# Optimization experiments

Hardware: AMD Instinct MI355X
Metric: run time of the kernel (lower is better)

Reference implementation:

```python
import jax, jax.numpy as jnp
import numpy as np

DIM = 1024
NUM_HEADS = 16
HEAD_DIM = DIM // NUM_HEADS
SCALE = HEAD_DIM ** -0.5


def setup_inputs() -> dict:
    key = jax.random.key(0)
    ks = jax.random.split(key, 6)
    B, N = 2, 2048
    s = DIM ** -0.5
    return {
        "x": jax.random.normal(ks[0], (B, N, DIM), dtype=jnp.float32),
        "Wq": jax.random.normal(ks[1], (DIM, DIM), dtype=jnp.float32) * s,
        "Wk": jax.random.normal(ks[2], (DIM, DIM), dtype=jnp.float32) * s,
        "Wv": jax.random.normal(ks[3], (DIM, DIM), dtype=jnp.float32) * s,
        "Wp": jax.random.normal(ks[4], (DIM, DIM), dtype=jnp.float32) * s,
        "bp": jax.random.normal(ks[5], (DIM,), dtype=jnp.float32) * 0.01,
    }


def reference(x, Wq, Wk, Wv, Wp, bp):
    B, N, C = x.shape
    H, D = NUM_HEADS, HEAD_DIM
    # projections (torch Linear: x @ W.T); reshape to (B, H, N, D)
    q = (x @ Wq.T).reshape(B, N, H, D).transpose(0, 2, 1, 3)
    k = (x @ Wk.T).reshape(B, N, H, D).transpose(0, 2, 1, 3)
    v = (x @ Wv.T).reshape(B, N, H, D).transpose(0, 2, 1, 3)
    attn = jnp.einsum("bhnd,bhmd->bhnm", q, k) * SCALE
    attn = jax.nn.softmax(attn, axis=-1)  # dropout p=0 -> identity
    out = jnp.einsum("bhnm,bhmd->bhnd", attn, v)
    out = out.transpose(0, 2, 1, 3).reshape(B, N, C)
    return out @ Wp.T + bp
```

## Files before the change

kernel.cpp:

```cpp
#include <hip/hip_runtime.h>
#include <cstdint>

#define DIMC   1024
#define NHEADS 16
#define HD     64
#define BATCH  2
#define SEQ    2048
#define MROWS  (BATCH*SEQ)
#define QSCALE2 0.18033688f

typedef __bf16 bf16x8 __attribute__((ext_vector_type(8)));
typedef float  f32x4  __attribute__((ext_vector_type(4)));

#define AST 88
#define TST 136

__device__ __forceinline__ unsigned short f2bf(float f) {
    union { float f; unsigned int u; } v; v.f = f;
    unsigned int u = v.u;
    u += 0x7fffu + ((u >> 16) & 1u);
    return (unsigned short)(u >> 16);
}

__device__ __forceinline__ unsigned int pk2bf(float a, float b) {
    union { float f; unsigned int u; } ua, ub;
    ua.f = a; ub.f = b;
    return __builtin_amdgcn_perm(ub.u + 0x8000u, ua.u + 0x8000u, 0x07060302u);
}

__device__ __forceinline__ void gload_lds16(const void* g, void* l) {
    __builtin_amdgcn_global_load_lds(
        (const __attribute__((address_space(1))) unsigned int*)g,
        (__attribute__((address_space(3))) unsigned int*)l, 16, 0, 0);
}

__global__ __launch_bounds__(256) void cast_all(
    const float* __restrict__ x,
    const float* __restrict__ Wq, const float* __restrict__ Wk,
    const float* __restrict__ Wv, const float* __restrict__ Wp,
    unsigned short* __restrict__ xb, unsigned short* __restrict__ Wb)
{
    const size_t M1 = (size_t)DIMC * DIMC;
    int y = blockIdx.y;
    const float* src;
    unsigned short* dst;
    if (y < 4)      { src = x  + (size_t)y * M1; dst = xb + (size_t)y * M1; }
    else if (y == 4){ src = Wq; dst = Wb; }
    else if (y == 5){ src = Wk; dst = Wb + M1; }
    else if (y == 6){ src = Wv; dst = Wb + 2 * M1; }
    else            { src = Wp; dst = Wb + 3 * M1; }
    size_t idx = ((size_t)blockIdx.x * 256 + threadIdx.x) * 4;
    float4 v = *(const float4*)(src + idx);
    ushort4 p; p.x = f2bf(v.x); p.y = f2bf(v.y); p.z = f2bf(v.z); p.w = f2bf(v.w);
    *(ushort4*)(dst + idx) = p;
}

__device__ __forceinline__ void gemm_issue(
    const unsigned short* __restrict__ A, const unsigned short* __restrict__ B,
    unsigned short* As, unsigned short* Bs, int m0, int n0, int kt)
{
    const int t = threadIdx.x;
    const int w = t >> 6, lane = t & 63;
    const int srow = lane >> 3, scol = lane & 7;
#pragma unroll
    for (int i = 0; i < 4; ++i) {
        int r  = i * 32 + w * 8 + srow;
        int cg = scol ^ (r & 7);
        gload_lds16(A + (size_t)(m0 + r) * DIMC + kt + cg * 8, As + r * 64 + scol * 8);
        gload_lds16(B + (size_t)(n0 + r) * DIMC + kt + cg * 8, Bs + r * 64 + scol * 8);
    }
}

__device__ __forceinline__ void gemm_compute(
    const unsigned short* As, const unsigned short* Bs, f32x4 acc[4][4])
{
    const int t = threadIdx.x;
    const int w = t >> 6, lane = t & 63, quad = lane >> 4, lr = lane & 15;
    const int wr = w >> 1, wc = w & 1;
#pragma unroll
    for (int kk = 0; kk < 2; ++kk) {
        bf16x8 af[4], bfr[4];
#pragma unroll
        for (int mt = 0; mt < 4; ++mt) {
            int row = wr * 64 + mt * 16 + lr;
            int cb  = kk * 4 + quad;
            af[mt] = *(const bf16x8*)&As[row * 64 + (cb ^ (row & 7)) * 8];
        }
#pragma unroll
        for (int nt = 0; nt < 4; ++nt) {
            int row = wc * 64 + nt * 16 + lr;
            int cb  = kk * 4 + quad;
            bfr[nt] = *(const bf16x8*)&Bs[row * 64 + (cb ^ (row & 7)) * 8];
        }
#pragma unroll
        for (int mt = 0; mt < 4; ++mt)
#pragma unroll
            for (int nt = 0; nt < 4; ++nt)
                acc[mt][nt] = __builtin_amdgcn_mfma_f32_16x16x32_bf16(af[mt], bfr[nt], acc[mt][nt], 0, 0, 0);
    }
}

__device__ __forceinline__ void gemm_k_loop_db(
    const unsigned short* __restrict__ A, const unsigned short* __restrict__ B,
    unsigned short* smem, int m0, int n0, f32x4 acc[4][4])
{
    unsigned short* As0 = smem;
    unsigned short* Bs0 = smem + 8192;
    unsigned short* As1 = smem + 16384;
    unsigned short* Bs1 = smem + 24576;

    gemm_issue(A, B, As0, Bs0, m0, n0, 0);
    for (int kt = 0; kt < DIMC; kt += 128) {
        __syncthreads();
        gemm_issue(A, B, As1, Bs1, m0, n0, kt + 64);
        gemm_compute(As0, Bs0, acc);
        __syncthreads();
        if (kt + 128 < DIMC) gemm_issue(A, B, As0, Bs0, m0, n0, kt + 128);
        gemm_compute(As1, Bs1, acc);
    }
}

__device__ __forceinline__ void vt_epilogue(
    unsigned short* Ts, f32x4 acc[4][4], int m0, int n0,
    unsigned short* __restrict__ vT)
{
    const int t = threadIdx.x;
    const int w = t >> 6, lane = t & 63, quad = lane >> 4, lr = lane & 15;
    const int wr = w >> 1, wc = w & 1;

    __syncthreads();
#pragma unroll
    for (int mt = 0; mt < 4; ++mt)
#pragma unroll
        for (int nt = 0; nt < 4; ++nt) {
            int lcol  = wc * 64 + nt * 16 + lr;
            int lrow0 = wr * 64 + mt * 16 + quad * 4;
            ushort4 p;
            p.x = f2bf(acc[mt][nt][0]); p.y = f2bf(acc[mt][nt][1]);
            p.z = f2bf(acc[mt][nt][2]); p.w = f2bf(acc[mt][nt][3]);
            *(ushort4*)&Ts[lcol * TST + lrow0] = p;
        }
    __syncthreads();

    int lc = t >> 1, half = t & 1;
    int cg = n0 + lc, hh = cg >> 6, dd = cg & 63;
    int bb = m0 >> 11, nn0 = m0 & (SEQ - 1);
    size_t dst = ((size_t)((bb * NHEADS + hh) * HD + dd)) * SEQ + nn0 + half * 64;
    const unsigned short* srcp = &Ts[lc * TST + half * 64];
#pragma unroll
    for (int i = 0; i < 8; ++i)
        *(uint4*)&vT[dst + i * 8] = *(const uint4*)&srcp[i * 8];
}

__global__ __launch_bounds__(256) void gemm_qkv_fast(
    const unsigned short* __restrict__ xb, const unsigned short* __restrict__ Wb,
    unsigned short* __restrict__ qo, unsigned short* __restrict__ ko,
    unsigned short* __restrict__ vT)
{
    __shared__ unsigned short smem[32768];

    const int t  = threadIdx.x;
    const int n0 = blockIdx.x * 128, m0 = blockIdx.y * 128, z = blockIdx.z;
    const unsigned short* B = Wb + (size_t)z * DIMC * DIMC;
    const int w = t >> 6, lane = t & 63, quad = lane >> 4, lr = lane & 15;
    const int wr = w >> 1, wc = w & 1;

    f32x4 acc[4][4];
#pragma unroll
    for (int mt = 0; mt < 4; ++mt)
#pragma unroll
        for (int nt = 0; nt < 4; ++nt)
#pragma unroll
            for (int r = 0; r < 4; ++r) acc[mt][nt][r] = 0.f;

    gemm_k_loop_db(xb, B, smem, m0, n0, acc);

    if (z == 2) {
        vt_epilogue(smem, acc, m0, n0, vT);
    } else {
        unsigned short* Out = (z == 0) ? qo : ko;
        const float sc = (z == 0) ? QSCALE2 : 1.0f;
#pragma unroll
        for (int mt = 0; mt < 4; ++mt)
#pragma unroll
            for (int nt = 0; nt < 4; ++nt)
#pragma unroll
                for (int r = 0; r < 4; ++r) {
                    int row = m0 + wr * 64 + mt * 16 + quad * 4 + r;
                    int col = n0 + wc * 64 + nt * 16 + lr;
                    Out[(size_t)row * DIMC + col] = f2bf(acc[mt][nt][r] * sc);
                }
    }
}

__global__ __launch_bounds__(256) void gemm_out_fast(
    const unsigned short* __restrict__ O, const unsigned short* __restrict__ Wpb,
    const float* __restrict__ bias, float* __restrict__ out)
{
    __shared__ unsigned short smem[32768];

    const int t  = threadIdx.x;
    const int n0 = blockIdx.x * 128, m0 = blockIdx.y * 128;
    const int w = t >> 6, lane = t & 63, quad = lane >> 4, lr = lane & 15;
    const int wr = w >> 1, wc = w & 1;

    f32x4 acc[4][4];
#pragma unroll
    for (int mt = 0; mt < 4; ++mt)
#pragma unroll
        for (int nt = 0; nt < 4; ++nt)
#pragma unroll
            for (int r = 0; r < 4; ++r) acc[mt][nt][r] = 0.f;

    gemm_k_loop_db(O, Wpb, smem, m0, n0, acc);

#pragma unroll
    for (int mt = 0; mt < 4; ++mt)
#pragma unroll
        for (int nt = 0; nt < 4; ++nt)
#pragma unroll
            for (int r = 0; r < 4; ++r) {
                int row = m0 + wr * 64 + mt * 16 + quad * 4 + r;
                int col = n0 + wc * 64 + nt * 16 + lr;
                out[(size_t)row * DIMC + col] = acc[mt][nt][r] + bias[col];
            }
}

__global__ __launch_bounds__(256, 4) void attn_kernel(
    const unsigned short* __restrict__ qg, const unsigned short* __restrict__ kg,
    const unsigned short* __restrict__ vT, unsigned short* __restrict__ og)
{
    __shared__ unsigned short Ka[64 * 64];
    __shared__ unsigned short Kb[64 * 64];
    __shared__ unsigned short Va[64 * 64];
    __shared__ unsigned short Vb[64 * 64];
    __shared__ unsigned short Ps[64 * 64];

    const int t  = threadIdx.x;
    const int w = t >> 6, l = t & 63, quad = l >> 4, lr = l & 15;
    const int srow = t >> 3, scol = t & 7;
    const int pkey = (lr & 7) << 1;

    const int bid  = blockIdx.x;
    const int slot = bid >> 3;
    const int bh   = (bid & 7) * 4 + (slot >> 5);
    const int qt   = slot & 31;
    const int b    = bh >> 4, h = bh & 15;

    const unsigned short* khead = kg + ((size_t)(b * SEQ)) * DIMC + h * HD;
    const unsigned short* vhead = vT + (size_t)((b * NHEADS + h) * HD) * SEQ;

    bf16x8 qf[2];
    {
        const size_t qoff = ((size_t)(b * SEQ + qt * 64 + w * 16 + lr)) * DIMC + h * HD;
        qf[0] = *(const bf16x8*)(qg + qoff + 0  + quad * 8);
        qf[1] = *(const bf16x8*)(qg + qoff + 32 + quad * 8);
    }

    bf16x8 ones;
#pragma unroll
    for (int j = 0; j < 8; ++j) ones[j] = (__bf16)1.0f;
    const f32x4 fzero = { 0.f, 0.f, 0.f, 0.f };

    f32x4 o_acc[4], lacc;
    lacc = fzero;
#pragma unroll
    for (int ct = 0; ct < 4; ++ct) o_acc[ct] = fzero;

    auto issue = [&](int kt, unsigned short* Kd, unsigned short* Vd) {
#pragma unroll
        for (int i = 0; i < 2; ++i) {
            int r  = i * 32 + srow;
            int cg = scol ^ (r & 7);
            gload_lds16(khead + (size_t)(kt * 64 + r) * DIMC + cg * 8, Kd + r * 64 + scol * 8);
            gload_lds16(vhead + (size_t)r * SEQ + kt * 64 + cg * 8,   Vd + r * 64 + scol * 8);
        }
    };

    auto phase = [&](const unsigned short* Kc, const unsigned short* Vc) {
        f32x4 s[4];
#pragma unroll
        for (int nt = 0; nt < 4; ++nt) {
            int row = nt * 16 + lr;
            bf16x8 kf = *(const bf16x8*)&Kc[row * 64 + ((quad ^ (row & 7)) * 8)];
            s[nt] = __builtin_amdgcn_mfma_f32_16x16x32_bf16(kf, qf[0], fzero, 0, 0, 0);
        }
#pragma unroll
        for (int nt = 0; nt < 4; ++nt) {
            int row = nt * 16 + lr;
            bf16x8 kf = *(const bf16x8*)&Kc[row * 64 + (((4 + quad) ^ (row & 7)) * 8)];
            s[nt] = __builtin_amdgcn_mfma_f32_16x16x32_bf16(kf, qf[1], s[nt], 0, 0, 0);
        }

#pragma unroll
        for (int nt = 0; nt < 4; ++nt) {
            uint2 pp;
            pp.x = pk2bf(__builtin_amdgcn_exp2f(s[nt][0]),
                         __builtin_amdgcn_exp2f(s[nt][1]));
            pp.y = pk2bf(__builtin_amdgcn_exp2f(s[nt][2]),
                         __builtin_amdgcn_exp2f(s[nt][3]));
            *(uint2*)&Ps[(w * 16 + lr) * 64 + (((nt * 4 + quad) ^ pkey) * 4)] = pp;
        }

#pragma unroll
        for (int kk = 0; kk < 2; ++kk) {
            bf16x8 vf[4];
#pragma unroll
            for (int ct = 0; ct < 4; ++ct) {
                int row = ct * 16 + lr;
                vf[ct] = *(const bf16x8*)&Vc[row * 64 + (((kk * 4 + quad) ^ (row & 7)) * 8)];
            }
            bf16x8 pf = *(const bf16x8*)&Ps[(w * 16 + lr) * 64 + (((kk * 8 + quad * 2) ^ pkey) * 4)];
            lacc = __builtin_amdgcn_mfma_f32_16x16x32_bf16(pf, ones, lacc, 0, 0, 0);
#pragma unroll
            for (int ct = 0; ct < 4; ++ct)
                o_acc[ct] = __builtin_amdgcn_mfma_f32_16x16x32_bf16(pf, vf[ct], o_acc[ct], 0, 0, 0);
        }
    };

    issue(0, Ka, Va);
    for (int kt = 0; kt < SEQ / 64; kt += 2) {
        __syncthreads();
        issue(kt + 1, Kb, Vb);
        phase(Ka, Va);
        __syncthreads();
        if (kt + 2 < SEQ / 64) issue(kt + 2, Ka, Va);
        phase(Kb, Vb);
    }

    {
        float inv[4];
#pragma unroll
        for (int r = 0; r < 4; ++r) inv[r] = 1.0f / lacc[r];
#pragma unroll
        for (int ct = 0; ct < 4; ++ct)
#pragma unroll
            for (int r = 0; r < 4; ++r) {
                int qrow = qt * 64 + w * 16 + quad * 4 + r;
                og[((size_t)(b * SEQ + qrow)) * DIMC + h * HD + ct * 16 + lr] =
                    f2bf(o_acc[ct][r] * inv[r]);
            }
    }
}

__global__ __launch_bounds__(256) void gemm_qkv_f32(
    const float* __restrict__ x,
    const float* __restrict__ Wq, const float* __restrict__ Wk, const float* __restrict__ Wv,
    unsigned short* __restrict__ qo, unsigned short* __restrict__ ko, unsigned short* __restrict__ vT)
{
    __shared__ unsigned short smem[2 * 128 * AST];
    unsigned short* As = smem;
    unsigned short* Bs = smem + 128 * AST;

    const int t  = threadIdx.x;
    const int n0 = blockIdx.x * 128, m0 = blockIdx.y * 128, z = blockIdx.z;
    const float* W = (z == 0) ? Wq : (z == 1) ? Wk : Wv;
    const int w = t >> 6, l = t & 63, quad = l >> 4, lr = l & 15;
    const int wr = w >> 1, wc = w & 1;

    f32x4 acc[4][4];
#pragma unroll
    for (int mt = 0; mt < 4; ++mt)
#pragma unroll
        for (int nt = 0; nt < 4; ++nt)
#pragma unroll
            for (int r = 0; r < 4; ++r) acc[mt][nt][r] = 0.f;

    for (int kt = 0; kt < DIMC; kt += 64) {
        __syncthreads();
#pragma unroll
        for (int i = 0; i < 8; ++i) {
            int flat = t + i * 256;
            int row = flat >> 4, seg = flat & 15;
            float4 a = *(const float4*)(x + (size_t)(m0 + row) * DIMC + kt + seg * 4);
            ushort4 pa; pa.x = f2bf(a.x); pa.y = f2bf(a.y); pa.z = f2bf(a.z); pa.w = f2bf(a.w);
            *(ushort4*)&As[row * AST + seg * 4] = pa;
            float4 b = *(const float4*)(W + (size_t)(n0 + row) * DIMC + kt + seg * 4);
            ushort4 pb; pb.x = f2bf(b.x); pb.y = f2bf(b.y); pb.z = f2bf(b.z); pb.w = f2bf(b.w);
            *(ushort4*)&Bs[row * AST + seg * 4] = pb;
        }
        __syncthreads();
#pragma unroll
        for (int kk = 0; kk < 2; ++kk) {
            bf16x8 af[4], bfr[4];
#pragma unroll
            for (int mt = 0; mt < 4; ++mt)
                af[mt] = *(const bf16x8*)&As[(wr * 64 + mt * 16 + lr) * AST + kk * 32 + quad * 8];
#pragma unroll
            for (int nt = 0; nt < 4; ++nt)
                bfr[nt] = *(const bf16x8*)&Bs[(wc * 64 + nt * 16 + lr) * AST + kk * 32 + quad * 8];
#pragma unroll
            for (int mt = 0; mt < 4; ++mt)
#pragma unroll
                for (int nt = 0; nt < 4; ++nt)
                    acc[mt][nt] = __builtin_amdgcn_mfma_f32_16x16x32_bf16(af[mt], bfr[nt], acc[mt][nt], 0, 0, 0);
        }
    }

    if (z == 2) {
        __syncthreads();
#pragma unroll
        for (int mt = 0; mt < 4; ++mt)
#pragma unroll
            for (int nt = 0; nt < 4; ++nt) {
                int lcol  = wc * 64 + nt * 16 + lr;
                int lrow0 = wr * 64 + mt * 16 + quad * 4;
                ushort4 p;
                p.x = f2bf(acc[mt][nt][0]); p.y = f2bf(acc[mt][nt][1]);
                p.z = f2bf(acc[mt][nt][2]); p.w = f2bf(acc[mt][nt][3]);
                *(ushort4*)&smem[lcol * TST + lrow0] = p;
            }
        __syncthreads();
        int lc = t >> 1, half = t & 1;
        int cg = n0 + lc, hh = cg >> 6, dd = cg & 63;
        int bb = m0 >> 11, nn0 = m0 & (SEQ - 1);
        size_t dst = ((size_t)((bb * NHEADS + hh) * HD + dd)) * SEQ + nn0 + half * 64;
        const unsigned short* srcp = &smem[lc * TST + half * 64];
#pragma unroll
        for (int i = 0; i < 8; ++i)
            *(uint4*)&vT[dst + i * 8] = *(const uint4*)&srcp[i * 8];
    } else {
        unsigned short* Out = (z == 0) ? qo : ko;
        const float sc = (z == 0) ? QSCALE2 : 1.0f;
#pragma unroll
        for (int mt = 0; mt < 4; ++mt)
#pragma unroll
            for (int nt = 0; nt < 4; ++nt)
#pragma unroll
                for (int r = 0; r < 4; ++r) {
                    int row = m0 + wr * 64 + mt * 16 + quad * 4 + r;
                    int col = n0 + wc * 64 + nt * 16 + lr;
                    Out[(size_t)row * DIMC + col] = f2bf(acc[mt][nt][r] * sc);
                }
    }
}

__global__ __launch_bounds__(256) void gemm_out_f32(
    const unsigned short* __restrict__ A, const float* __restrict__ Wp,
    const float* __restrict__ bias, float* __restrict__ out)
{
    __shared__ unsigned short As[128 * AST];
    __shared__ unsigned short Bs[128 * AST];

    const int t  = threadIdx.x;
    const int n0 = blockIdx.x * 128, m0 = blockIdx.y * 128;
    const int w = t >> 6, l = t & 63, quad = l >> 4, lr = l & 15;
    const int wr = w >> 1, wc = w & 1;

    f32x4 acc[4][4];
#pragma unroll
    for (int mt = 0; mt < 4; ++mt)
#pragma unroll
        for (int nt = 0; nt < 4; ++nt)
#pragma unroll
            for (int r = 0; r < 4; ++r) acc[mt][nt][r] = 0.f;

    for (int kt = 0; kt < DIMC; kt += 64) {
        __syncthreads();
#pragma unroll
        for (int i = 0; i < 8; ++i) {
            int flat = t + i * 256;
            int row = flat >> 4, seg = flat & 15;
            ushort4 a = *(const ushort4*)(A + (size_t)(m0 + row) * DIMC + kt + seg * 4);
            *(ushort4*)&As[row * AST + seg * 4] = a;
            float4 b = *(const float4*)(Wp + (size_t)(n0 + row) * DIMC + kt + seg * 4);
            ushort4 pb; pb.x = f2bf(b.x); pb.y = f2bf(b.y); pb.z = f2bf(b.z); pb.w = f2bf(b.w);
            *(ushort4*)&Bs[row * AST + seg * 4] = pb;
        }
        __syncthreads();
#pragma unroll
        for (int kk = 0; kk < 2; ++kk) {
            bf16x8 af[4], bfr[4];
#pragma unroll
            for (int mt = 0; mt < 4; ++mt)
                af[mt] = *(const bf16x8*)&As[(wr * 64 + mt * 16 + lr) * AST + kk * 32 + quad * 8];
#pragma unroll
            for (int nt = 0; nt < 4; ++nt)
                bfr[nt] = *(const bf16x8*)&Bs[(wc * 64 + nt * 16 + lr) * AST + kk * 32 + quad * 8];
#pragma unroll
            for (int mt = 0; mt < 4; ++mt)
#pragma unroll
                for (int nt = 0; nt < 4; ++nt)
                    acc[mt][nt] = __builtin_amdgcn_mfma_f32_16x16x32_bf16(af[mt], bfr[nt], acc[mt][nt], 0, 0, 0);
        }
    }

#pragma unroll
    for (int mt = 0; mt < 4; ++mt)
#pragma unroll
        for (int nt = 0; nt < 4; ++nt)
#pragma unroll
            for (int r = 0; r < 4; ++r) {
                int row = m0 + wr * 64 + mt * 16 + quad * 4 + r;
                int col = n0 + wc * 64 + nt * 16 + lr;
                out[(size_t)row * DIMC + col] = acc[mt][nt][r] + bias[col];
            }
}

extern "C" void kernel_launch(void* const* d_in, const int* in_sizes, int n_in,
                              void* d_out, int out_size, void* d_ws, size_t ws_size,
                              hipStream_t stream)
{
    const float* x  = (const float*)d_in[0];
    const float* Wq = (const float*)d_in[1];
    const float* Wk = (const float*)d_in[2];
    const float* Wv = (const float*)d_in[3];
    const float* Wp = (const float*)d_in[4];
    const float* bp = (const float*)d_in[5];
    float* out = (float*)d_out;

    const size_t SZ  = (size_t)MROWS * DIMC;
    const size_t WSZ = (size_t)DIMC * DIMC;
    const size_t need = (4 * SZ + 4 * WSZ) * sizeof(unsigned short);

    if (ws_size >= need) {
        unsigned short* q  = (unsigned short*)d_ws;
        unsigned short* k  = q + SZ;
        unsigned short* vt = k + SZ;
        unsigned short* o  = vt + SZ;
        unsigned short* Wb = o + SZ;
        unsigned short* xb = (unsigned short*)d_out;

        cast_all<<<dim3(1024, 8), 256, 0, stream>>>(x, Wq, Wk, Wv, Wp, xb, Wb);
        gemm_qkv_fast<<<dim3(DIMC / 128, MROWS / 128, 3), 256, 0, stream>>>(xb, Wb, q, k, vt);
        attn_kernel<<<dim3(1024), 256, 0, stream>>>(q, k, vt, o);
        gemm_out_fast<<<dim3(DIMC / 128, MROWS / 128), 256, 0, stream>>>(o, Wb + 3 * WSZ, bp, out);
    } else {
        unsigned short* q  = (unsigned short*)d_ws;
        unsigned short* k  = q + SZ;
        unsigned short* vt = k + SZ;
        unsigned short* o  = vt + SZ;

        gemm_qkv_f32<<<dim3(DIMC / 128, MROWS / 128, 3), 256, 0, stream>>>(x, Wq, Wk, Wv, q, k, vt);
        attn_kernel<<<dim3(1024), 256, 0, stream>>>(q, k, vt, o);
        gemm_out_f32<<<dim3(DIMC / 128, MROWS / 128), 256, 0, stream>>>(o, Wp, bp, out);
    }
}
```

Measured before the change: 182.7 us.

## Switch attention to 32x32x16 MFMA with split-KV waves and LDS merge

The attention kernel now uses 32x32x16 bf16 MFMA instead of 16x16x32. Each wave owns 32 query rows and half of each 64-key tile, so two waves split the KV dimension. The partial outputs and row sums are then merged through LDS at the end. The aim is fewer MFMA instructions and fewer LDS fragment loads per tile, at the cost of an extra synchronized reduction step and a different P-tile layout per wave.

Measured after the change: 197.3 us. 8.0% more time.

```diff
diff --git a/kernel.cpp b/kernel.cpp
--- a/kernel.cpp
+++ b/kernel.cpp
@@ -11,6 +11,7 @@
 
 typedef __bf16 bf16x8 __attribute__((ext_vector_type(8)));
 typedef float  f32x4  __attribute__((ext_vector_type(4)));
+typedef float  f32x16 __attribute__((ext_vector_type(16)));
 
 #define AST 88
 #define TST 136
@@ -230,16 +231,21 @@
     const unsigned short* __restrict__ qg, const unsigned short* __restrict__ kg,
     const unsigned short* __restrict__ vT, unsigned short* __restrict__ og)
 {
-    __shared__ unsigned short Ka[64 * 64];
-    __shared__ unsigned short Kb[64 * 64];
-    __shared__ unsigned short Va[64 * 64];
-    __shared__ unsigned short Vb[64 * 64];
-    __shared__ unsigned short Ps[64 * 64];
+    __shared__ unsigned short smem[20480];
+    unsigned short* Ka = smem;
+    unsigned short* Kb = smem + 4096;
+    unsigned short* Va = smem + 8192;
+    unsigned short* Vb = smem + 12288;
+    unsigned short* Ps = smem + 16384;
 
     const int t  = threadIdx.x;
-    const int w = t >> 6, l = t & 63, quad = l >> 4, lr = l & 15;
+    const int w = t >> 6, l = t & 63;
+    const int col = l & 31, hi = l >> 5;
+    const int qh = w >> 1, kvh = w & 1;
     const int srow = t >> 3, scol = t & 7;
-    const int pkey = (lr & 7) << 1;
+    const int pkey = (col & 3) << 1;
+
+    unsigned short* PsW = Ps + w * 1024;
 
     const int bid  = blockIdx.x;
     const int slot = bid >> 3;
@@ -250,22 +256,21 @@
     const unsigned short* khead = kg + ((size_t)(b * SEQ)) * DIMC + h * HD;
     const unsigned short* vhead = vT + (size_t)((b * NHEADS + h) * HD) * SEQ;
 
-    bf16x8 qf[2];
+    bf16x8 qf[4];
     {
-        const size_t qoff = ((size_t)(b * SEQ + qt * 64 + w * 16 + lr)) * DIMC + h * HD;
-        qf[0] = *(const bf16x8*)(qg + qoff + 0  + quad * 8);
-        qf[1] = *(const bf16x8*)(qg + qoff + 32 + quad * 8);
+        const size_t qoff = ((size_t)(b * SEQ + qt * 64 + qh * 32 + col)) * DIMC + h * HD + hi * 8;
+#pragma unroll
+        for (int ks = 0; ks < 4; ++ks)
+            qf[ks] = *(const bf16x8*)(qg + qoff + ks * 16);
     }
 
     bf16x8 ones;
 #pragma unroll
     for (int j = 0; j < 8; ++j) ones[j] = (__bf16)1.0f;
-    const f32x4 fzero = { 0.f, 0.f, 0.f, 0.f };
-
-    f32x4 o_acc[4], lacc;
-    lacc = fzero;
-#pragma unroll
-    for (int ct = 0; ct < 4; ++ct) o_acc[ct] = fzero;
+
+    f32x16 o0, o1, lac;
+#pragma unroll
+    for (int r = 0; r < 16; ++r) { o0[r] = 0.f; o1[r] = 0.f; lac[r] = 0.f; }
 
     auto issue = [&](int kt, unsigned short* Kd, unsigned short* Vd) {
 #pragma unroll
@@ -278,44 +283,48 @@
     };
 
     auto phase = [&](const unsigned short* Kc, const unsigned short* Vc) {
-        f32x4 s[4];
-#pragma unroll
-        for (int nt = 0; nt < 4; ++nt) {
-            int row = nt * 16 + lr;
-            bf16x8 kf = *(const bf16x8*)&Kc[row * 64 + ((quad ^ (row & 7)) * 8)];
-            s[nt] = __builtin_amdgcn_mfma_f32_16x16x32_bf16(kf, qf[0], fzero, 0, 0, 0);
-        }
-#pragma unroll
-        for (int nt = 0; nt < 4; ++nt) {
-            int row = nt * 16 + lr;
-            bf16x8 kf = *(const bf16x8*)&Kc[row * 64 + (((4 + quad) ^ (row & 7)) * 8)];
-            s[nt] = __builtin_amdgcn_mfma_f32_16x16x32_bf16(kf, qf[1], s[nt], 0, 0, 0);
-        }
-
-#pragma unroll
-        for (int nt = 0; nt < 4; ++nt) {
-            uint2 pp;
-            pp.x = pk2bf(__builtin_amdgcn_exp2f(s[nt][0]),
-                         __builtin_amdgcn_exp2f(s[nt][1]));
-            pp.y = pk2bf(__builtin_amdgcn_exp2f(s[nt][2]),
-                         __builtin_amdgcn_exp2f(s[nt][3]));
-            *(uint2*)&Ps[(w * 16 + lr) * 64 + (((nt * 4 + quad) ^ pkey) * 4)] = pp;
-        }
-
-#pragma unroll
-        for (int kk = 0; kk < 2; ++kk) {
-            bf16x8 vf[4];
-#pragma unroll
-            for (int ct = 0; ct < 4; ++ct) {
-                int row = ct * 16 + lr;
-                vf[ct] = *(const bf16x8*)&Vc[row * 64 + (((kk * 4 + quad) ^ (row & 7)) * 8)];
+        f32x16 s;
+#pragma unroll
+        for (int r = 0; r < 16; ++r) s[r] = 0.f;
+#pragma unroll
+        for (int ks = 0; ks < 4; ++ks) {
+            int r = kvh * 32 + col;
+            int c = ks * 2 + hi;
+            bf16x8 kf = *(const bf16x8*)&Kc[r * 64 + ((c ^ (r & 7)) * 8)];
+            s = __builtin_amdgcn_mfma_f32_32x32x16_bf16(kf, qf[ks], s, 0, 0, 0);
+        }
+
+        bf16x8 vf[2][2];
+#pragma unroll
+        for (int dt = 0; dt < 2; ++dt)
+#pragma unroll
+            for (int ks2 = 0; ks2 < 2; ++ks2) {
+                int r = dt * 32 + col;
+                int c = kvh * 4 + ks2 * 2 + hi;
+                vf[dt][ks2] = *(const bf16x8*)&Vc[r * 64 + ((c ^ (r & 7)) * 8)];
             }
-            bf16x8 pf = *(const bf16x8*)&Ps[(w * 16 + lr) * 64 + (((kk * 8 + quad * 2) ^ pkey) * 4)];
-            lacc = __builtin_amdgcn_mfma_f32_16x16x32_bf16(pf, ones, lacc, 0, 0, 0);
-#pragma unroll
-            for (int ct = 0; ct < 4; ++ct)
-                o_acc[ct] = __builtin_amdgcn_mfma_f32_16x16x32_bf16(pf, vf[ct], o_acc[ct], 0, 0, 0);
-        }
+
+        unsigned int pk[8];
+#pragma unroll
+        for (int i = 0; i < 8; ++i)
+            pk[i] = pk2bf(__builtin_amdgcn_exp2f(s[2 * i]),
+                          __builtin_amdgcn_exp2f(s[2 * i + 1]));
+#pragma unroll
+        for (int i2 = 0; i2 < 4; ++i2) {
+            int cw = i2 * 2 + hi;
+            uint2 pp; pp.x = pk[2 * i2]; pp.y = pk[2 * i2 + 1];
+            *(uint2*)&PsW[col * 32 + ((cw ^ pkey) << 2)] = pp;
+        }
+
+        bf16x8 pf0 = *(const bf16x8*)&PsW[col * 32 + (((2 * hi) ^ pkey) << 2)];
+        bf16x8 pf1 = *(const bf16x8*)&PsW[col * 32 + (((4 + 2 * hi) ^ pkey) << 2)];
+
+        lac = __builtin_amdgcn_mfma_f32_32x32x16_bf16(pf0, ones, lac, 0, 0, 0);
+        lac = __builtin_amdgcn_mfma_f32_32x32x16_bf16(pf1, ones, lac, 0, 0, 0);
+        o0  = __builtin_amdgcn_mfma_f32_32x32x16_bf16(pf0, vf[0][0], o0, 0, 0, 0);
+        o0  = __builtin_amdgcn_mfma_f32_32x32x16_bf16(pf1, vf[0][1], o0, 0, 0, 0);
+        o1  = __builtin_amdgcn_mfma_f32_32x32x16_bf16(pf0, vf[1][0], o1, 0, 0, 0);
+        o1  = __builtin_amdgcn_mfma_f32_32x32x16_bf16(pf1, vf[1][1], o1, 0, 0, 0);
     };
 
     issue(0, Ka, Va);
@@ -328,18 +337,31 @@
         phase(Kb, Vb);
     }
 
-    {
-        float inv[4];
-#pragma unroll
-        for (int r = 0; r < 4; ++r) inv[r] = 1.0f / lacc[r];
-#pragma unroll
-        for (int ct = 0; ct < 4; ++ct)
-#pragma unroll
-            for (int r = 0; r < 4; ++r) {
-                int qrow = qt * 64 + w * 16 + quad * 4 + r;
-                og[((size_t)(b * SEQ + qrow)) * DIMC + h * HD + ct * 16 + lr] =
-                    f2bf(o_acc[ct][r] * inv[r]);
-            }
+    __syncthreads();
+    float* mrg = (float*)smem;
+    if (kvh == 1) {
+        float* dst = mrg + (qh * 64 + l) * 49;
+#pragma unroll
+        for (int r = 0; r < 16; ++r) {
+            dst[r] = o0[r]; dst[16 + r] = o1[r]; dst[32 + r] = lac[r];
+        }
+    }
+    __syncthreads();
+    if (kvh == 0) {
+        const float* src = mrg + (qh * 64 + l) * 49;
+        float inv[16];
+#pragma unroll
+        for (int r = 0; r < 16; ++r) {
+            o0[r] += src[r]; o1[r] += src[16 + r];
+            inv[r] = 1.0f / (lac[r] + src[32 + r]);
+        }
+#pragma unroll
+        for (int r = 0; r < 16; ++r) {
+            int qrow = qt * 64 + qh * 32 + (r & 3) + 8 * (r >> 2) + 4 * hi;
+            size_t base = ((size_t)(b * SEQ + qrow)) * DIMC + h * HD;
+            og[base + col]      = f2bf(o0[r] * inv[r]);
+            og[base + 32 + col] = f2bf(o1[r] * inv[r]);
+        }
     }
 }
 
```
